# Performance work log

Measured on AMD Instinct MI355X. Metric: run time of the kernel, lower is better.

Reference implementation:

```python
import jax, jax.numpy as jnp
import numpy as np

NUM_GROUPS = 32
EPS = 1e-5

def group_norm(x, weight, bias):
    # x: [B, C, H, W]
    b, c, h, w = x.shape
    g = NUM_GROUPS
    xg = x.reshape(b, g, (c // g) * h * w)
    mean = xg.mean(axis=-1, keepdims=True)
    var = xg.var(axis=-1, keepdims=True)
    xn = ((xg - mean) * jax.lax.rsqrt(var + EPS)).reshape(b, c, h, w)
    return xn * weight[None, :, None, None] + bias[None, :, None, None]

def setup_inputs() -> dict:
    key = jax.random.key(0)
    ks = jax.random.split(key, 4)
    B, C, H, W = 4, 256, 64, 64
    x = jax.random.normal(ks[0], (B, C, H, W), dtype=jnp.float32)
    gn_weight = jnp.ones((C,), dtype=jnp.float32)
    gn_bias = jnp.zeros((C,), dtype=jnp.float32)
    # 1x1 conv == linear over channel dim; init ~ kaiming-uniform-ish scale
    qkv_weight = jax.random.normal(ks[1], (3 * C, C), dtype=jnp.float32) / np.sqrt(C)
    qkv_bias = jnp.zeros((3 * C,), dtype=jnp.float32)
    out_weight = jax.random.normal(ks[2], (C, C), dtype=jnp.float32) / np.sqrt(C)
    out_bias = jnp.zeros((C,), dtype=jnp.float32)
    return {"x": x, "gn_weight": gn_weight, "gn_bias": gn_bias,
            "qkv_weight": qkv_weight, "qkv_bias": qkv_bias,
            "out_weight": out_weight, "out_bias": out_bias}

def reference(x, gn_weight, gn_bias, qkv_weight, qkv_bias, out_weight, out_bias):
    b, c, h, w = x.shape
    n = h * w
    xn = group_norm(x, gn_weight, gn_bias)
    # 1x1 conv QKV projection: [B, 3C, H, W]
    qkv = jnp.einsum('bchw,oc->bohw', xn, qkv_weight) + qkv_bias[None, :, None, None]
    q, k, v = jnp.split(qkv, 3, axis=1)
    q = q.transpose(0, 2, 3, 1).reshape(b, n, c)   # [B, N, C]
    k = k.reshape(b, c, n)                         # [B, C, N]
    v = v.transpose(0, 2, 3, 1).reshape(b, n, c)   # [B, N, C]
    scores = jnp.einsum('bnc,bcm->bnm', q, k) * (c ** -0.5)  # [B, N, N]
    attn = jax.nn.softmax(scores, axis=-1)
    out = jnp.einsum('bnm,bmc->bnc', attn, v)      # [B, N, C]
    out = out.reshape(b, h, w, c).transpose(0, 3, 1, 2)  # [B, C, H, W]
    out = jnp.einsum('bchw,oc->bohw', out, out_weight) + out_bias[None, :, None, None]
    return out + x
```

## Files before the change

### kernel.cpp

```cpp
#include <hip/hip_runtime.h>
#include <math.h>

#define B_   4
#define C_   256
#define G_   32
#define CPG  8
#define N_   4096
#define NPG  (CPG * N_)
#define EPS  1e-5f
#define SCALE 0.0625f
#define NCH  32

typedef __attribute__((ext_vector_type(8)))  __bf16 bf16x8;
typedef __attribute__((ext_vector_type(4)))  __bf16 bf16x4;
typedef __attribute__((ext_vector_type(16))) float  f32x16;

__global__ __launch_bounds__(256) void gn_stats_kernel(const float* __restrict__ x,
                                                       float* __restrict__ part) {
    int bid = blockIdx.x;
    int bg = bid >> 2, seg = bid & 3;
    const float4* xp4 = (const float4*)(x + (size_t)bg * NPG) + seg * 2048;
    int tid = threadIdx.x;

    float s = 0.f, ss = 0.f;
    for (int i = tid; i < 2048; i += 256) {
        float4 t = xp4[i];
        s  += t.x + t.y + t.z + t.w;
        ss += t.x * t.x + t.y * t.y + t.z * t.z + t.w * t.w;
    }
    #pragma unroll
    for (int off = 32; off; off >>= 1) {
        s  += __shfl_xor(s, off, 64);
        ss += __shfl_xor(ss, off, 64);
    }
    __shared__ float rs[2][4];
    int wave = tid >> 6, lane = tid & 63;
    if (lane == 0) { rs[0][wave] = s; rs[1][wave] = ss; }
    __syncthreads();
    if (tid == 0) {
        part[bid * 2]     = rs[0][0] + rs[0][1] + rs[0][2] + rs[0][3];
        part[bid * 2 + 1] = rs[1][0] + rs[1][1] + rs[1][2] + rs[1][3];
    }
}

__global__ __launch_bounds__(256) void gn_apply_kernel(const float* __restrict__ x,
                                                       const float* __restrict__ w,
                                                       const float* __restrict__ bia,
                                                       const float* __restrict__ part,
                                                       __bf16* __restrict__ xnb) {
    int bid = blockIdx.x;
    int b   = (bid & 7) >> 1;
    int u   = ((bid >> 3) << 1) | (bid & 1);
    int g   = u >> 4;
    int seg = u & 15;
    int bg  = b * 32 + g;
    float s  = part[(bg * 4 + 0) * 2] + part[(bg * 4 + 1) * 2]
             + part[(bg * 4 + 2) * 2] + part[(bg * 4 + 3) * 2];
    float ss = part[(bg * 4 + 0) * 2 + 1] + part[(bg * 4 + 1) * 2 + 1]
             + part[(bg * 4 + 2) * 2 + 1] + part[(bg * 4 + 3) * 2 + 1];
    float mean = s / (float)NPG;
    float var  = ss / (float)NPG - mean * mean;
    float rstd = rsqrtf(var + EPS);

    const float* xp = x + (size_t)bg * NPG;
    int n = seg * 256 + threadIdx.x;

    bf16x8 pk;
    #pragma unroll
    for (int cc = 0; cc < 8; cc++) {
        float sc = rstd * w[g * CPG + cc];
        float sh = bia[g * CPG + cc] - mean * sc;
        pk[cc] = (__bf16)(xp[(size_t)cc * N_ + n] * sc + sh);
    }
    size_t idx = ((((size_t)(b * 128 + (n >> 5)) * 16 + (g >> 1)) * 2 + (g & 1))
                  * 32 + (n & 31)) * 8;
    *(bf16x8*)(xnb + idx) = pk;
}

__global__ __launch_bounds__(256) void qkv_kernel(const __bf16* __restrict__ xnb,
                                                  const float* __restrict__ W,
                                                  const float* __restrict__ bias,
                                                  __bf16* __restrict__ q,
                                                  __bf16* __restrict__ k,
                                                  __bf16* __restrict__ v) {
    int bid = blockIdx.x;
    int b   = (bid & 7) >> 1;
    int t2  = ((bid >> 3) << 1) | (bid & 1);
    int ot  = t2 >> 5;
    int nc  = t2 & 31;
    int tid = threadIdx.x, wv = tid >> 6, lane = tid & 63;
    int n31 = lane & 31, q2 = lane >> 5;
    int B0 = ot * 128 + wv * 32;

    bf16x8 wf[16];
    const float* wp = W + (size_t)(B0 + n31) * C_;
    #pragma unroll
    for (int ks = 0; ks < 16; ks++) {
        float4 t0 = *(const float4*)(wp + ks * 16 + q2 * 8);
        float4 t1 = *(const float4*)(wp + ks * 16 + q2 * 8 + 4);
        bf16x8 f;
        f[0] = (__bf16)t0.x; f[1] = (__bf16)t0.y; f[2] = (__bf16)t0.z; f[3] = (__bf16)t0.w;
        f[4] = (__bf16)t1.x; f[5] = (__bf16)t1.y; f[6] = (__bf16)t1.z; f[7] = (__bf16)t1.w;
        wf[ks] = f;
    }

    float bv[16], bvv = 0.f;
    if (ot < 4) {
        #pragma unroll
        for (int gI = 0; gI < 4; gI++)
            #pragma unroll
            for (int j = 0; j < 4; j++)
                bv[gI * 4 + j] = bias[B0 + gI * 8 + 4 * q2 + j];
    } else {
        bvv = bias[B0 + n31];
    }

    const __bf16* xb = xnb + (size_t)b * 128 * 8192;

    for (int t = 0; t < 4; t++) {
        int nt = nc * 4 + t;
        const __bf16* xg = xb + (size_t)nt * 8192 + q2 * 256 + n31 * 8;
        bf16x8 xf[16];
        #pragma unroll
        for (int ks = 0; ks < 16; ks++) xf[ks] = *(const bf16x8*)(xg + ks * 512);

        f32x16 acc;
        #pragma unroll
        for (int i = 0; i < 16; i++) acc[i] = 0.f;
        if (ot < 4) {
            #pragma unroll
            for (int ks = 0; ks < 16; ks++)
                acc = __builtin_amdgcn_mfma_f32_32x32x16_bf16(wf[ks], xf[ks], acc, 0, 0, 0);
        } else {
            #pragma unroll
            for (int ks = 0; ks < 16; ks++)
                acc = __builtin_amdgcn_mfma_f32_32x32x16_bf16(xf[ks], wf[ks], acc, 0, 0, 0);
        }

        if (ot < 4) {
            int ocb = (ot < 2) ? B0 : (B0 - 256);
            __bf16* dst = (ot < 2) ? q : k;
            bool isq = (ot < 2);
            #pragma unroll
            for (int gI = 0; gI < 4; gI++) {
                bf16x4 pk;
                #pragma unroll
                for (int j = 0; j < 4; j++) {
                    float y = acc[gI * 4 + j] + bv[gI * 4 + j];
                    if (isq) y *= SCALE;
                    pk[j] = (__bf16)y;
                }
                size_t idx = ((((size_t)(b * 128 + nt) * 16 + ((ocb >> 4) + (gI >> 1))) * 2
                               + (gI & 1)) * 32 + n31) * 8 + 4 * q2;
                *(bf16x4*)(dst + idx) = pk;
            }
        } else {
            int ocb = B0 - 512;
            #pragma unroll
            for (int gI = 0; gI < 4; gI++) {
                bf16x4 pk;
                #pragma unroll
                for (int j = 0; j < 4; j++)
                    pk[j] = (__bf16)(acc[gI * 4 + j] + bvv);
                size_t idx = (((((size_t)(b * 128 + nt) * 2 + (gI >> 1)) * 2 + (gI & 1)) * 8
                               + (ocb >> 5)) * 32 + n31) * 8 + 4 * q2;
                *(bf16x4*)(v + idx) = pk;
            }
        }
    }
}

__device__ __forceinline__ void stage16(const __bf16* g, __bf16* l) {
    __builtin_amdgcn_global_load_lds(
        (const __attribute__((address_space(1))) unsigned int*)g,
        (__attribute__((address_space(3))) unsigned int*)l, 16, 0, 0);
}

__global__ __launch_bounds__(512, 4) void attn_kernel(const __bf16* __restrict__ q,
                                                      const __bf16* __restrict__ k,
                                                      const __bf16* __restrict__ v,
                                                      __bf16* __restrict__ aob,
                                                      float* __restrict__ lpart,
                                                      float* __restrict__ ltmp) {
    __shared__ __align__(16) __bf16 k_lds[2][16384];
    __shared__ __align__(16) __bf16 p_lds[2][64 * 64];

    int bid   = blockIdx.x;
    int xcd   = bid & 7;
    int b     = xcd >> 1;
    int split = xcd & 1;
    int qt    = bid >> 3;
    int n0    = qt * 64;

    int tid = threadIdx.x;
    int wid = tid >> 6, lane = tid & 63;
    int n31 = lane & 31, q2 = lane >> 5;

    const size_t BSTR = (size_t)N_ * C_;
    const size_t PLANE = (size_t)B_ * C_ * N_;
    float* lt = ltmp + (size_t)bid * 128;
    const __bf16* kgbase = k + (size_t)(b * 128 + split * 64) * 8192
                           + wid * 2048 + lane * 8;

    {
        __bf16* l = (__bf16*)k_lds[0] + wid * 2048;
        #pragma unroll
        for (int i = 0; i < 4; i++)
            stage16(kgbase + i * 512, l + i * 512);
    }

    if (wid < 4) {
        int kt = wid & 1;
        int rt = wid >> 1;
        const __bf16* qg = q + (size_t)(b * 128 + qt * 2 + rt) * 8192
                           + q2 * 256 + n31 * 8;
        bf16x8 qf[16];
        #pragma unroll
        for (int ks = 0; ks < 16; ks++) qf[ks] = *(const bf16x8*)(qg + ks * 512);

        float l_acc = 0.f;
        int prow = rt * 32 + n31;
        int swz  = (prow & 7) << 4;
        int klo  = kt * 8192 + q2 * 256 + n31 * 8;

        for (int ch = 0; ch < NCH; ch++) {
            __syncthreads();
            if (ch < NCH - 1) {
                const __bf16* g = kgbase + (size_t)(ch + 1) * 16384;
                __bf16* l = (__bf16*)k_lds[(ch + 1) & 1] + wid * 2048;
                #pragma unroll
                for (int i = 0; i < 4; i++)
                    stage16(g + i * 512, l + i * 512);
            }
            const __bf16* kl = (const __bf16*)k_lds[ch & 1] + klo;
            f32x16 sa, sb;
            #pragma unroll
            for (int i = 0; i < 16; i++) { sa[i] = 0.f; sb[i] = 0.f; }
            __builtin_amdgcn_s_setprio(1);
            #pragma unroll
            for (int i = 0; i < 8; i++) {
                bf16x8 ka = *(const bf16x8*)(kl + i * 512);
                bf16x8 kb = *(const bf16x8*)(kl + (i + 8) * 512);
                sa = __builtin_amdgcn_mfma_f32_32x32x16_bf16(ka, qf[i], sa, 0, 0, 0);
                sb = __builtin_amdgcn_mfma_f32_32x32x16_bf16(kb, qf[i + 8], sb, 0, 0, 0);
            }
            __builtin_amdgcn_s_setprio(0);
            char* pbuf = (char*)p_lds[ch & 1];
            #pragma unroll
            for (int gI = 0; gI < 4; gI++) {
                bf16x4 pw;
                #pragma unroll
                for (int j = 0; j < 4; j++) {
                    float p = __expf(sa[gI * 4 + j] + sb[gI * 4 + j]);
                    l_acc += p;
                    pw[j] = (__bf16)p;
                }
                int off = prow * 128 + kt * 64 + 16 * gI + 8 * q2;
                *(bf16x4*)(pbuf + (off ^ swz)) = pw;
            }
        }
        l_acc += __shfl_down(l_acc, 32);
        if (lane < 32) lt[kt * 64 + rt * 32 + lane] = l_acc;
        __syncthreads();
    } else {
        int cw = wid - 4;
        const __bf16* vbase = v + (size_t)b * BSTR + (size_t)split * 524288
                              + (size_t)q2 * 2048 + n31 * 8;
        f32x16 o_acc[2][2];
        #pragma unroll
        for (int ct = 0; ct < 2; ct++)
            #pragma unroll
            for (int rt = 0; rt < 2; rt++)
                #pragma unroll
                for (int i = 0; i < 16; i++) o_acc[ct][rt][i] = 0.f;

        for (int ch = 0; ch < NCH; ch++) {
            __syncthreads();
            if (ch < NCH - 1) {
                const __bf16* g = kgbase + (size_t)(ch + 1) * 16384;
                __bf16* l = (__bf16*)k_lds[(ch + 1) & 1] + wid * 2048;
                #pragma unroll
                for (int i = 0; i < 4; i++)
                    stage16(g + i * 512, l + i * 512);
            }
            if (ch > 0) {
                int cc = ch - 1;
                bf16x8 vf[2][4];
                #pragma unroll
                for (int ct = 0; ct < 2; ct++)
                    #pragma unroll
                    for (int ks4 = 0; ks4 < 4; ks4++) {
                        size_t off = (size_t)(cc * 2 + (ks4 >> 1)) * 8192
                                   + (size_t)(ks4 & 1) * 4096 + (cw * 2 + ct) * 256;
                        vf[ct][ks4] = *(const bf16x8*)(vbase + off);
                    }
                const char* pbuf = (const char*)p_lds[cc & 1];
                __builtin_amdgcn_s_setprio(1);
                #pragma unroll
                for (int rt = 0; rt < 2; rt++) {
                    int prow = rt * 32 + n31;
                    int swz  = (prow & 7) << 4;
                    int pbs  = prow * 128 + q2 * 16;
                    #pragma unroll
                    for (int ks4 = 0; ks4 < 4; ks4++) {
                        bf16x8 pf = *(const bf16x8*)(pbuf + ((pbs + ks4 * 32) ^ swz));
                        o_acc[0][rt] = __builtin_amdgcn_mfma_f32_32x32x16_bf16(
                            vf[0][ks4], pf, o_acc[0][rt], 0, 0, 0);
                        o_acc[1][rt] = __builtin_amdgcn_mfma_f32_32x32x16_bf16(
                            vf[1][ks4], pf, o_acc[1][rt], 0, 0, 0);
                    }
                }
                __builtin_amdgcn_s_setprio(0);
            }
        }
        __syncthreads();
        float lA = lt[n31] + lt[64 + n31];
        float lB = lt[32 + n31] + lt[64 + 32 + n31];
        {
            int cc = NCH - 1;
            bf16x8 vf[2][4];
            #pragma unroll
            for (int ct = 0; ct < 2; ct++)
                #pragma unroll
                for (int ks4 = 0; ks4 < 4; ks4++) {
                    size_t off = (size_t)(cc * 2 + (ks4 >> 1)) * 8192
                               + (size_t)(ks4 & 1) * 4096 + (cw * 2 + ct) * 256;
                    vf[ct][ks4] = *(const bf16x8*)(vbase + off);
                }
            const char* pbuf = (const char*)p_lds[1];
            __builtin_amdgcn_s_setprio(1);
            #pragma unroll
            for (int rt = 0; rt < 2; rt++) {
                int prow = rt * 32 + n31;
                int swz  = (prow & 7) << 4;
                int pbs  = prow * 128 + q2 * 16;
                #pragma unroll
                for (int ks4 = 0; ks4 < 4; ks4++) {
                    bf16x8 pf = *(const bf16x8*)(pbuf + ((pbs + ks4 * 32) ^ swz));
                    o_acc[0][rt] = __builtin_amdgcn_mfma_f32_32x32x16_bf16(
                        vf[0][ks4], pf, o_acc[0][rt], 0, 0, 0);
                    o_acc[1][rt] = __builtin_amdgcn_mfma_f32_32x32x16_bf16(
                        vf[1][ks4], pf, o_acc[1][rt], 0, 0, 0);
                }
            }
            __builtin_amdgcn_s_setprio(0);
        }
        if (wid == 4 && lane < 32) {
            float* lp = lpart + ((size_t)split * B_ + b) * N_ + n0;
            lp[n31]      = lA;
            lp[32 + n31] = lB;
        }
        float inv0 = 1.0f / lA;
        float inv1 = 1.0f / lB;
        __bf16* aop = aob + (size_t)split * PLANE;
        #pragma unroll
        for (int ct = 0; ct < 2; ct++)
            #pragma unroll
            for (int rt = 0; rt < 2; rt++) {
                float inv = rt ? inv1 : inv0;
                #pragma unroll
                for (int g = 0; g < 4; g++) {
                    bf16x4 st;
                    #pragma unroll
                    for (int j = 0; j < 4; j++)
                        st[j] = (__bf16)(o_acc[ct][rt][g * 4 + j] * inv);
                    size_t idx = ((((((size_t)(b * 64 + qt) * 4 + cw) * 2 + ct) * 2 + rt)
                                   * 4 + g) * 2 + q2) * 128 + n31 * 4;
                    *(bf16x4*)(aop + idx) = st;
                }
            }
    }
}

__global__ __launch_bounds__(256) void proj_kernel(const __bf16* __restrict__ aob,
                                                   const float* __restrict__ lpart,
                                                   const float* __restrict__ W2,
                                                   const float* __restrict__ bias,
                                                   const float* __restrict__ x,
                                                   float* __restrict__ out) {
    int bid = blockIdx.x;
    int b   = (bid & 7) >> 1;
    int u   = ((bid >> 3) << 1) | (bid & 1);
    int ot  = u >> 5;
    int nc  = u & 31;
    int tid = threadIdx.x, wv = tid >> 6, lane = tid & 63;
    int n31 = lane & 31, q2 = lane >> 5;
    int B0 = ot * 128 + wv * 32;
    const size_t BN = (size_t)B_ * N_;
    const size_t PLANE = (size_t)B_ * C_ * N_;

    bf16x8 wf[16];
    const float* wp = W2 + (size_t)(B0 + n31) * C_;
    #pragma unroll
    for (int ks = 0; ks < 16; ks++) {
        float4 t0 = *(const float4*)(wp + ks * 16 + q2 * 8);
        float4 t1 = *(const float4*)(wp + ks * 16 + q2 * 8 + 4);
        bf16x8 f;
        f[0] = (__bf16)t0.x; f[1] = (__bf16)t0.y; f[2] = (__bf16)t0.z; f[3] = (__bf16)t0.w;
        f[4] = (__bf16)t1.x; f[5] = (__bf16)t1.y; f[6] = (__bf16)t1.z; f[7] = (__bf16)t1.w;
        wf[ks] = f;
    }
    float bv[16];
    #pragma unroll
    for (int r = 0; r < 16; r++) bv[r] = bias[B0 + (r & 3) + 8 * (r >> 2) + 4 * q2];

    for (int t = 0; t < 4; t++) {
        int nt = nc * 4 + t;
        int qt = nt >> 1, rtile = nt & 1;
        int n = nt * 32 + n31;
        size_t ln = (size_t)b * N_ + n;
        float l0v = lpart[ln];
        float l1v = lpart[BN + ln];
        float invt = 1.0f / (l0v + l1v);
        float w0 = l0v * invt, w1 = l1v * invt;

        bf16x8 xf[16];
        #pragma unroll
        for (int ks = 0; ks < 16; ks++) {
            int oct = ks * 2 + q2;
            int cw = oct >> 3, ct = (oct >> 2) & 1, ga = oct & 3;
            size_t base = ((((((size_t)(b * 64 + qt) * 4 + cw) * 2 + ct) * 2 + rtile)
                            * 4 + ga) * 2) * 128 + n31 * 4;
            bf16x4 a0 = *(const bf16x4*)(aob + base);
            bf16x4 b0 = *(const bf16x4*)(aob + base + 128);
            bf16x4 a1 = *(const bf16x4*)(aob + PLANE + base);
            bf16x4 b1 = *(const bf16x4*)(aob + PLANE + base + 128);
            bf16x8 f;
            #pragma unroll
            for (int j = 0; j < 4; j++) {
                f[j]     = (__bf16)(w0 * (float)a0[j] + w1 * (float)a1[j]);
                f[4 + j] = (__bf16)(w0 * (float)b0[j] + w1 * (float)b1[j]);
            }
            xf[ks] = f;
        }

        f32x16 acc;
        #pragma unroll
        for (int i = 0; i < 16; i++) acc[i] = 0.f;
        #pragma unroll
        for (int ks = 0; ks < 16; ks++)
            acc = __builtin_amdgcn_mfma_f32_32x32x16_bf16(wf[ks], xf[ks], acc, 0, 0, 0);

        #pragma unroll
        for (int r = 0; r < 16; r++) {
            int o = B0 + (r & 3) + 8 * (r >> 2) + 4 * q2;
            size_t idx = ((size_t)(b * C_ + o)) * N_ + nt * 32 + n31;
            out[idx] = acc[r] + bv[r] + x[idx];
        }
    }
}

extern "C" void kernel_launch(void* const* d_in, const int* in_sizes, int n_in,
                              void* d_out, int out_size, void* d_ws, size_t ws_size,
                              hipStream_t stream) {
    const float* x     = (const float*)d_in[0];
    const float* gn_w  = (const float*)d_in[1];
    const float* gn_b  = (const float*)d_in[2];
    const float* qkv_w = (const float*)d_in[3];
    const float* qkv_b = (const float*)d_in[4];
    const float* out_w = (const float*)d_in[5];
    const float* out_b = (const float*)d_in[6];
    float* out = (float*)d_out;

    const size_t SZ = (size_t)B_ * C_ * N_;
    char* base = (char*)d_ws;
    __bf16* aob = (__bf16*)base;
    __bf16* xnb = (__bf16*)base;
    __bf16* qb  = (__bf16*)(base + 2 * SZ * 4);
    __bf16* kb  = qb + SZ;
    __bf16* vb  = kb + SZ;
    float*  lpart = (float*)(base + 2 * SZ * 4 + 3 * SZ * 2);
    float*  part  = lpart + 2 * (size_t)B_ * N_;
    float*  ltmp  = part + 1024;

    gn_stats_kernel<<<dim3(512), 256, 0, stream>>>(x, part);
    gn_apply_kernel<<<dim3(2048), 256, 0, stream>>>(x, gn_w, gn_b, part, xnb);
    qkv_kernel<<<dim3(768), 256, 0, stream>>>(xnb, qkv_w, qkv_b, qb, kb, vb);
    attn_kernel<<<dim3(512), 512, 0, stream>>>(qb, kb, vb, aob, lpart, ltmp);
    proj_kernel<<<dim3(256), 256, 0, stream>>>(aob, lpart, out_w, out_b, x, out);
}
```

Measured before the change: 209.2 us.

## Vectorize groupnorm apply, LDS double-buffer QKV input, split proj grid

gn_apply now has each thread load float4 runs across 8 channels and write four packed bf16x8 outputs, so the grid shrinks from 2048 to 512 blocks. qkv_kernel stages its normalized input tiles into double-buffered LDS with global_load_lds, prefetching the next tile while the current one is consumed, so the four waves share one copy instead of each reading global memory. proj_kernel processes two column tiles per block instead of four and doubles the grid to 512 blocks for more parallelism. The costs are extra barriers and LDS use in qkv, and the weights are reloaded twice as often in proj.

```diff
diff --git a/kernel.cpp b/kernel.cpp
--- a/kernel.cpp
+++ b/kernel.cpp
@@ -15,6 +15,12 @@
 typedef __attribute__((ext_vector_type(4)))  __bf16 bf16x4;
 typedef __attribute__((ext_vector_type(16))) float  f32x16;
 
+__device__ __forceinline__ void stage16(const __bf16* g, __bf16* l) {
+    __builtin_amdgcn_global_load_lds(
+        (const __attribute__((address_space(1))) unsigned int*)g,
+        (__attribute__((address_space(3))) unsigned int*)l, 16, 0, 0);
+}
+
 __global__ __launch_bounds__(256) void gn_stats_kernel(const float* __restrict__ x,
                                                        float* __restrict__ part) {
     int bid = blockIdx.x;
@@ -51,8 +57,8 @@
     int bid = blockIdx.x;
     int b   = (bid & 7) >> 1;
     int u   = ((bid >> 3) << 1) | (bid & 1);
-    int g   = u >> 4;
-    int seg = u & 15;
+    int g   = u >> 2;
+    int seg = u & 3;
     int bg  = b * 32 + g;
     float s  = part[(bg * 4 + 0) * 2] + part[(bg * 4 + 1) * 2]
              + part[(bg * 4 + 2) * 2] + part[(bg * 4 + 3) * 2];
@@ -63,18 +69,32 @@
     float rstd = rsqrtf(var + EPS);
 
     const float* xp = x + (size_t)bg * NPG;
-    int n = seg * 256 + threadIdx.x;
-
-    bf16x8 pk;
+    int n0 = seg * 1024 + threadIdx.x * 4;
+
+    float4 t[8];
+    #pragma unroll
+    for (int cc = 0; cc < 8; cc++)
+        t[cc] = *(const float4*)(xp + (size_t)cc * N_ + n0);
+
+    float sc[8], sh[8];
     #pragma unroll
     for (int cc = 0; cc < 8; cc++) {
-        float sc = rstd * w[g * CPG + cc];
-        float sh = bia[g * CPG + cc] - mean * sc;
-        pk[cc] = (__bf16)(xp[(size_t)cc * N_ + n] * sc + sh);
-    }
-    size_t idx = ((((size_t)(b * 128 + (n >> 5)) * 16 + (g >> 1)) * 2 + (g & 1))
-                  * 32 + (n & 31)) * 8;
-    *(bf16x8*)(xnb + idx) = pk;
+        sc[cc] = rstd * w[g * CPG + cc];
+        sh[cc] = bia[g * CPG + cc] - mean * sc[cc];
+    }
+
+    size_t base = ((((size_t)(b * 128 + (n0 >> 5)) * 16 + (g >> 1)) * 2 + (g & 1))
+                   * 32 + (n0 & 31)) * 8;
+    #pragma unroll
+    for (int j = 0; j < 4; j++) {
+        bf16x8 pk;
+        #pragma unroll
+        for (int cc = 0; cc < 8; cc++) {
+            float tv = ((const float*)&t[cc])[j];
+            pk[cc] = (__bf16)(tv * sc[cc] + sh[cc]);
+        }
+        *(bf16x8*)(xnb + base + j * 8) = pk;
+    }
 }
 
 __global__ __launch_bounds__(256) void qkv_kernel(const __bf16* __restrict__ xnb,
@@ -83,6 +103,7 @@
                                                   __bf16* __restrict__ q,
                                                   __bf16* __restrict__ k,
                                                   __bf16* __restrict__ v) {
+    __shared__ __align__(16) __bf16 x_lds[2][8192];
     int bid = blockIdx.x;
     int b   = (bid & 7) >> 1;
     int t2  = ((bid >> 3) << 1) | (bid & 1);
@@ -116,13 +137,29 @@
     }
 
     const __bf16* xb = xnb + (size_t)b * 128 * 8192;
+    const __bf16* xgs = xb + (size_t)(nc * 4) * 8192 + wv * 2048 + lane * 8;
+
+    {
+        __bf16* l = (__bf16*)x_lds[0] + wv * 2048;
+        #pragma unroll
+        for (int i = 0; i < 4; i++)
+            stage16(xgs + i * 512, l + i * 512);
+    }
 
     for (int t = 0; t < 4; t++) {
+        __syncthreads();
+        if (t < 3) {
+            const __bf16* g_ = xgs + (size_t)(t + 1) * 8192;
+            __bf16* l = (__bf16*)x_lds[(t + 1) & 1] + wv * 2048;
+            #pragma unroll
+            for (int i = 0; i < 4; i++)
+                stage16(g_ + i * 512, l + i * 512);
+        }
         int nt = nc * 4 + t;
-        const __bf16* xg = xb + (size_t)nt * 8192 + q2 * 256 + n31 * 8;
+        const __bf16* xl = (const __bf16*)x_lds[t & 1] + q2 * 256 + n31 * 8;
         bf16x8 xf[16];
         #pragma unroll
-        for (int ks = 0; ks < 16; ks++) xf[ks] = *(const bf16x8*)(xg + ks * 512);
+        for (int ks = 0; ks < 16; ks++) xf[ks] = *(const bf16x8*)(xl + ks * 512);
 
         f32x16 acc;
         #pragma unroll
@@ -168,12 +205,6 @@
             }
         }
     }
-}
-
-__device__ __forceinline__ void stage16(const __bf16* g, __bf16* l) {
-    __builtin_amdgcn_global_load_lds(
-        (const __attribute__((address_space(1))) unsigned int*)g,
-        (__attribute__((address_space(3))) unsigned int*)l, 16, 0, 0);
 }
 
 __global__ __launch_bounds__(512, 4) void attn_kernel(const __bf16* __restrict__ q,
@@ -381,8 +412,8 @@
     int bid = blockIdx.x;
     int b   = (bid & 7) >> 1;
     int u   = ((bid >> 3) << 1) | (bid & 1);
-    int ot  = u >> 5;
-    int nc  = u & 31;
+    int ot  = u >> 6;
+    int tp  = u & 63;
     int tid = threadIdx.x, wv = tid >> 6, lane = tid & 63;
     int n31 = lane & 31, q2 = lane >> 5;
     int B0 = ot * 128 + wv * 32;
@@ -404,8 +435,8 @@
     #pragma unroll
     for (int r = 0; r < 16; r++) bv[r] = bias[B0 + (r & 3) + 8 * (r >> 2) + 4 * q2];
 
-    for (int t = 0; t < 4; t++) {
-        int nt = nc * 4 + t;
+    for (int t = 0; t < 2; t++) {
+        int nt = tp * 2 + t;
         int qt = nt >> 1, rtile = nt & 1;
         int n = nt * 32 + n31;
         size_t ln = (size_t)b * N_ + n;
@@ -474,8 +505,8 @@
     float*  ltmp  = part + 1024;
 
     gn_stats_kernel<<<dim3(512), 256, 0, stream>>>(x, part);
-    gn_apply_kernel<<<dim3(2048), 256, 0, stream>>>(x, gn_w, gn_b, part, xnb);
+    gn_apply_kernel<<<dim3(512), 256, 0, stream>>>(x, gn_w, gn_b, part, xnb);
     qkv_kernel<<<dim3(768), 256, 0, stream>>>(xnb, qkv_w, qkv_b, qb, kb, vb);
     attn_kernel<<<dim3(512), 512, 0, stream>>>(qb, kb, vb, aob, lpart, ltmp);
-    proj_kernel<<<dim3(256), 256, 0, stream>>>(aob, lpart, out_w, out_b, x, out);
-}
+    proj_kernel<<<dim3(512), 256, 0, stream>>>(aob, lpart, out_w, out_b, x, out);
+}
```

Measured after the change: 205.0 us. -2.0%, faster.
